# Performance work log

Hardware: AMD Instinct MI355X
Metric: run time of the kernel (lower is better)

## Reference

```python
import jax, jax.numpy as jnp
import numpy as np

N_NODES = 50000
N_EDGES = 500000
IN_F, HID, EMB = 128, 256, 128

def setup_inputs() -> dict:
    key = jax.random.key(0)
    ks = jax.random.split(key, 9)
    x = jax.random.normal(ks[0], (N_NODES, IN_F), dtype=jnp.float32)
    src = jax.random.randint(ks[1], (N_EDGES,), 0, N_NODES, dtype=jnp.int32)
    dst = jax.random.randint(ks[2], (N_EDGES,), 0, N_NODES, dtype=jnp.int32)
    def lin(k, fan_in, fan_out):
        bound = 1.0 / np.sqrt(fan_in)
        kw, kb = jax.random.split(k)
        W = jax.random.uniform(kw, (fan_in, fan_out), minval=-bound, maxval=bound, dtype=jnp.float32)
        b = jax.random.uniform(kb, (fan_out,), minval=-bound, maxval=bound, dtype=jnp.float32)
        return W, b
    W1, b1 = lin(ks[3], IN_F, HID)
    W2, b2 = lin(ks[4], HID, HID)
    W3, b3 = lin(ks[5], HID, EMB)
    return {"x": x, "src": src, "dst": dst, "W1": W1, "b1": b1,
            "W2": W2, "b2": b2, "W3": W3, "b3": b3}

def _gcn_layer(h, src, dst, W, b):
    # sum messages from src nodes into dst nodes, then linear
    agg = jax.ops.segment_sum(h[src], dst, num_segments=N_NODES)  # [N, F]
    return agg @ W + b

def reference(x, src, dst, W1, b1, W2, b2, W3, b3):
    h = jax.nn.relu(_gcn_layer(x, src, dst, W1, b1))
    h = jax.nn.relu(_gcn_layer(h, src, dst, W2, b2))
    h = _gcn_layer(h, src, dst, W3, b3)
    # dgl.mean_nodes on a single graph: mean of relu(h) over all nodes -> [EMB]
    return jnp.mean(jax.nn.relu(h), axis=0)
```

## Files before the change

kernel.cpp:

```cpp
#include <hip/hip_runtime.h>

#define N_NODES 50000
#define N_EDGES 500000

typedef __attribute__((ext_vector_type(8))) short short8;
typedef __attribute__((ext_vector_type(4))) float floatx4;

__device__ inline float bf2f(unsigned short u) {
    unsigned int x = ((unsigned int)u) << 16;
    return __builtin_bit_cast(float, x);
}
__device__ inline unsigned short f2bf(float f) {
    unsigned int x = __builtin_bit_cast(unsigned int, f);
    x += 0x7fff + ((x >> 16) & 1);
    return (unsigned short)(x >> 16);
}


__global__ void hist_kernel(const int* __restrict__ dst, int* __restrict__ deg, int nE) {
    int e = blockIdx.x * 256 + threadIdx.x;
    if (e < nE) atomicAdd(&deg[dst[e]], 1);
}

__global__ void scan_block_kernel(const int* __restrict__ deg, int* __restrict__ partial,
                                  int* __restrict__ bsum, int n) {
    __shared__ int s[256];
    int i = blockIdx.x * 256 + threadIdx.x;
    int v = (i < n) ? deg[i] : 0;
    s[threadIdx.x] = v;
    __syncthreads();
    #pragma unroll
    for (int d = 1; d < 256; d <<= 1) {
        int t = (threadIdx.x >= d) ? s[threadIdx.x - d] : 0;
        __syncthreads();
        s[threadIdx.x] += t;
        __syncthreads();
    }
    if (i < n) partial[i] = s[threadIdx.x];
    if (threadIdx.x == 255) bsum[blockIdx.x] = s[255];
}

__global__ void scan_bsum_kernel(int* __restrict__ bsum, int nb) {
    __shared__ int s[256];
    int t = threadIdx.x;
    int v = (t < nb) ? bsum[t] : 0;
    s[t] = v;
    __syncthreads();
    #pragma unroll
    for (int d = 1; d < 256; d <<= 1) {
        int u = (t >= d) ? s[t - d] : 0;
        __syncthreads();
        s[t] += u;
        __syncthreads();
    }
    if (t < nb) bsum[t] = s[t];
}

__global__ void finalize_kernel(const int* __restrict__ partial, const int* __restrict__ bsum,
                                int* __restrict__ cur, int* __restrict__ off, int n) {
    int i = blockIdx.x * 256 + threadIdx.x;
    if (i == 0) off[0] = 0;
    if (i < n) {
        int base = (blockIdx.x > 0) ? bsum[blockIdx.x - 1] : 0;
        int incl = base + partial[i];
        off[i + 1] = incl;
        cur[i] = incl - cur[i];
    }
}

__global__ void fill_kernel(const int* __restrict__ src, const int* __restrict__ dst,
                            int* __restrict__ cur, int* __restrict__ csr, int nE) {
    int e = blockIdx.x * 256 + threadIdx.x;
    if (e < nE) {
        int p = atomicAdd(&cur[dst[e]], 1);
        csr[p] = src[e];
    }
}


__global__ __launch_bounds__(256) void prep_kernel(const float* __restrict__ W1,
                                                   const float* __restrict__ W2,
                                                   const float* __restrict__ W3,
                                                   const float* __restrict__ x,
                                                   unsigned short* __restrict__ Wt1,
                                                   unsigned short* __restrict__ Wt2,
                                                   unsigned short* __restrict__ Wt3,
                                                   unsigned short* __restrict__ xb) {
    int idx = blockIdx.x * 256 + threadIdx.x;
    if (idx < 32768) {
        int k = idx >> 8, n = idx & 255;
        Wt1[n * 128 + k] = f2bf(W1[idx]);
    } else if (idx < 98304) {
        int i = idx - 32768;
        int k = i >> 8, n = i & 255;
        Wt2[n * 256 + k] = f2bf(W2[i]);
    } else if (idx < 131072) {
        int i = idx - 98304;
        int k = i >> 7, n = i & 127;
        Wt3[n * 256 + k] = f2bf(W3[i]);
    } else {
        int i = (idx - 131072) * 4;
        if (i < N_NODES * 128) {
            float4 v = *(const float4*)(x + i);
            ushort4 o;
            o.x = f2bf(v.x); o.y = f2bf(v.y); o.z = f2bf(v.z); o.w = f2bf(v.w);
            *(ushort4*)(xb + i) = o;
        }
    }
}


__global__ __launch_bounds__(256) void agg256_kernel(const unsigned short* __restrict__ h,
                                                     const int* __restrict__ off,
                                                     const int* __restrict__ csr,
                                                     unsigned short* __restrict__ outp) {
    int wave = threadIdx.x >> 6, lane = threadIdx.x & 63;
    int node = blockIdx.x * 4 + wave;
    int f0 = lane * 4;
    int s = __builtin_amdgcn_readfirstlane(off[node]);
    int e = __builtin_amdgcn_readfirstlane(off[node + 1]);
    float a0 = 0.f, a1 = 0.f, a2 = 0.f, a3 = 0.f;
    int i = s;
    for (; i + 8 <= e; i += 8) {
        ushort4 r[8];
        #pragma unroll
        for (int j = 0; j < 8; j++) {
            int id = csr[i + j];
            r[j] = *(const ushort4*)(h + (size_t)id * 256 + f0);
        }
        #pragma unroll
        for (int j = 0; j < 8; j++) {
            a0 += bf2f(r[j].x); a1 += bf2f(r[j].y);
            a2 += bf2f(r[j].z); a3 += bf2f(r[j].w);
        }
    }
    if (i < e) {
        ushort4 r[8];
        #pragma unroll
        for (int j = 0; j < 8; j++) {
            int ii = i + j;
            int id = csr[ii < e ? ii : e - 1];
            r[j] = *(const ushort4*)(h + (size_t)id * 256 + f0);
        }
        #pragma unroll
        for (int j = 0; j < 8; j++) {
            if (i + j < e) {
                a0 += bf2f(r[j].x); a1 += bf2f(r[j].y);
                a2 += bf2f(r[j].z); a3 += bf2f(r[j].w);
            }
        }
    }
    ushort4 o;
    o.x = f2bf(a0); o.y = f2bf(a1); o.z = f2bf(a2); o.w = f2bf(a3);
    *(ushort4*)(outp + (size_t)node * 256 + f0) = o;
}


__device__ inline void agg128_body(const unsigned short* __restrict__ h,
                                   const int* __restrict__ off,
                                   const int* __restrict__ csr,
                                   int node, int half, int f0,
                                   float& a0, float& a1, float& a2, float& a3) {
    int s = __builtin_amdgcn_readfirstlane(off[node]);
    int e = __builtin_amdgcn_readfirstlane(off[node + 1]);
    int i = s;
    for (; i + 8 <= e; i += 8) {
        ushort4 r[4];
        #pragma unroll
        for (int j = 0; j < 4; j++) {
            int i0 = csr[i + 2 * j];
            int i1 = csr[i + 2 * j + 1];
            int id = half ? i1 : i0;
            r[j] = *(const ushort4*)(h + (size_t)id * 128 + f0);
        }
        #pragma unroll
        for (int j = 0; j < 4; j++) {
            a0 += bf2f(r[j].x); a1 += bf2f(r[j].y);
            a2 += bf2f(r[j].z); a3 += bf2f(r[j].w);
        }
    }
    if (i < e) {
        ushort4 r[4];
        #pragma unroll
        for (int j = 0; j < 4; j++) {
            int c0 = i + 2 * j     < e ? i + 2 * j     : e - 1;
            int c1 = i + 2 * j + 1 < e ? i + 2 * j + 1 : e - 1;
            int i0 = csr[c0];
            int i1 = csr[c1];
            int id = half ? i1 : i0;
            r[j] = *(const ushort4*)(h + (size_t)id * 128 + f0);
        }
        #pragma unroll
        for (int j = 0; j < 4; j++) {
            if (i + 2 * j + half < e) {
                a0 += bf2f(r[j].x); a1 += bf2f(r[j].y);
                a2 += bf2f(r[j].z); a3 += bf2f(r[j].w);
            }
        }
    }
    a0 += __shfl_xor(a0, 32, 64);
    a1 += __shfl_xor(a1, 32, 64);
    a2 += __shfl_xor(a2, 32, 64);
    a3 += __shfl_xor(a3, 32, 64);
}

__global__ __launch_bounds__(256) void agg128_kernel(const unsigned short* __restrict__ h,
                                                     const int* __restrict__ off,
                                                     const int* __restrict__ csr,
                                                     unsigned short* __restrict__ outp) {
    int wave = threadIdx.x >> 6, lane = threadIdx.x & 63;
    int node = blockIdx.x * 4 + wave;
    int half = lane >> 5;
    int f0 = (lane & 31) * 4;
    float a0, a1, a2, a3;
    a0 = a1 = a2 = a3 = 0.f;
    agg128_body(h, off, csr, node, half, f0, a0, a1, a2, a3);
    if (half == 0) {
        ushort4 o;
        o.x = f2bf(a0); o.y = f2bf(a1); o.z = f2bf(a2); o.w = f2bf(a3);
        *(ushort4*)(outp + (size_t)node * 128 + f0) = o;
    }
}


__global__ __launch_bounds__(256) void agg3_mean_kernel(const unsigned short* __restrict__ t,
                                                        const int* __restrict__ off,
                                                        const int* __restrict__ csr,
                                                        const float* __restrict__ b3,
                                                        float* __restrict__ partial) {
    __shared__ float sm[4 * 128];
    int wave = threadIdx.x >> 6, lane = threadIdx.x & 63;
    int node = blockIdx.x * 4 + wave;
    int half = lane >> 5;
    int f0 = (lane & 31) * 4;
    float a0, a1, a2, a3;
    a0 = a1 = a2 = a3 = 0.f;
    agg128_body(t, off, csr, node, half, f0, a0, a1, a2, a3);
    if (half == 0) {
        float4 bias = *(const float4*)(b3 + f0);
        float4 v;
        v.x = fmaxf(a0 + bias.x, 0.f);
        v.y = fmaxf(a1 + bias.y, 0.f);
        v.z = fmaxf(a2 + bias.z, 0.f);
        v.w = fmaxf(a3 + bias.w, 0.f);
        *(float4*)&sm[wave * 128 + f0] = v;
    }
    __syncthreads();
    if (threadIdx.x < 128) {
        int f = threadIdx.x;
        float p = sm[f] + sm[128 + f] + sm[256 + f] + sm[384 + f];
        partial[(size_t)blockIdx.x * 128 + f] = p;
    }
}

__global__ __launch_bounds__(256) void mean_reduce_kernel(const float* __restrict__ partial,
                                                          float* __restrict__ outp, int nRows) {
    __shared__ float s[256];
    int f = threadIdx.x & 127, half = threadIdx.x >> 7;
    int chunk = (nRows + gridDim.x - 1) / gridDim.x;
    int r0 = blockIdx.x * chunk;
    int r1 = r0 + chunk < nRows ? r0 + chunk : nRows;
    float acc = 0.f;
    for (int r = r0 + half; r < r1; r += 2) acc += partial[(size_t)r * 128 + f];
    s[threadIdx.x] = acc;
    __syncthreads();
    if (half == 0) atomicAdd(&outp[f], (s[f] + s[f + 128]) * (1.0f / N_NODES));
}


template<typename T> __device__ inline void storeC(T* p, float v);
template<> __device__ inline void storeC<float>(float* p, float v) { *p = v; }
template<> __device__ inline void storeC<unsigned short>(unsigned short* p, float v) { *p = f2bf(v); }

template<typename OUT_T>
__global__ __launch_bounds__(256) void gemm_bf16_kernel(const unsigned short* __restrict__ A,
                                                        const unsigned short* __restrict__ Bt,
                                                        const float* __restrict__ bias,
                                                        OUT_T* __restrict__ C,
                                                        int M, int K, int N, int doRelu) {
    constexpr int BM = 128, BN = 128, BK = 32, LDA = BK + 8;
    __shared__ unsigned short As[BM * LDA];
    __shared__ unsigned short Bs[BN * LDA];
    int tid = threadIdx.x;
    int m0 = blockIdx.y * BM, n0 = blockIdx.x * BN;
    int wave = tid >> 6, lane = tid & 63;
    int wm = wave >> 1, wn = wave & 1;
    int mlane = lane & 15, kgrp = lane >> 4;

    floatx4 acc[4][4];
    #pragma unroll
    for (int i = 0; i < 4; i++)
        #pragma unroll
        for (int j = 0; j < 4; j++) acc[i][j] = (floatx4){0.f, 0.f, 0.f, 0.f};

    for (int k0 = 0; k0 < K; k0 += BK) {
        #pragma unroll
        for (int it = 0; it < 2; ++it) {
            int c = tid + it * 256;
            int r = c >> 2, cb = (c & 3) * 8;
            int rg = m0 + r;
            short8 v;
            if (rg < M) v = *(const short8*)(A + (size_t)rg * K + k0 + cb);
            else        v = (short8){0, 0, 0, 0, 0, 0, 0, 0};
            *(short8*)&As[r * LDA + cb] = v;
            short8 w = *(const short8*)(Bt + (size_t)(n0 + r) * K + k0 + cb);
            *(short8*)&Bs[r * LDA + cb] = w;
        }
        __syncthreads();
        short8 af[4], bfr[4];
        #pragma unroll
        for (int mt = 0; mt < 4; mt++)
            af[mt] = *(const short8*)&As[(wm * 64 + mt * 16 + mlane) * LDA + kgrp * 8];
        #pragma unroll
        for (int nt = 0; nt < 4; nt++)
            bfr[nt] = *(const short8*)&Bs[(wn * 64 + nt * 16 + mlane) * LDA + kgrp * 8];
        #pragma unroll
        for (int mt = 0; mt < 4; mt++)
            #pragma unroll
            for (int nt = 0; nt < 4; nt++)
                acc[mt][nt] = __builtin_amdgcn_mfma_f32_16x16x32_bf16(af[mt], bfr[nt],
                                                                      acc[mt][nt], 0, 0, 0);
        __syncthreads();
    }
    #pragma unroll
    for (int mt = 0; mt < 4; mt++) {
        #pragma unroll
        for (int nt = 0; nt < 4; nt++) {
            int col = n0 + wn * 64 + nt * 16 + mlane;
            float bv = bias ? bias[col] : 0.f;
            #pragma unroll
            for (int r = 0; r < 4; r++) {
                int row = m0 + wm * 64 + mt * 16 + kgrp * 4 + r;
                if (row < M) {
                    float v = acc[mt][nt][r] + bv;
                    if (doRelu) v = fmaxf(v, 0.f);
                    storeC(C + (size_t)row * N + col, v);
                }
            }
        }
    }
}


extern "C" void kernel_launch(void* const* d_in, const int* in_sizes, int n_in,
                              void* d_out, int out_size, void* d_ws, size_t ws_size,
                              hipStream_t stream) {
    const float* x   = (const float*)d_in[0];
    const int*   src = (const int*)d_in[1];
    const int*   dst = (const int*)d_in[2];
    const float* W1 = (const float*)d_in[3];
    const float* b1 = (const float*)d_in[4];
    const float* W2 = (const float*)d_in[5];
    const float* b2 = (const float*)d_in[6];
    const float* W3 = (const float*)d_in[7];
    const float* b3 = (const float*)d_in[8];
    float* out = (float*)d_out;

    char* ws = (char*)d_ws;
    size_t o = 0;
    auto alloc = [&](size_t bytes) -> char* {
        char* p = ws + o;
        o = (o + bytes + 255) & ~(size_t)255;
        return p;
    };
    int* off     = (int*)alloc((size_t)(N_NODES + 1) * 4);
    int* cur     = (int*)alloc((size_t)N_NODES * 4);
    int* csr     = (int*)alloc((size_t)N_EDGES * 4);
    int* partial = (int*)alloc((size_t)N_NODES * 4);
    int* bsum    = (int*)alloc(256 * 4);
    unsigned short* Wt1 = (unsigned short*)alloc((size_t)128 * 256 * 2);
    unsigned short* Wt2 = (unsigned short*)alloc((size_t)256 * 256 * 2);
    unsigned short* Wt3 = (unsigned short*)alloc((size_t)256 * 128 * 2);
    char* R1 = alloc((size_t)N_NODES * 256 * 2);
    char* R2 = alloc((size_t)N_NODES * 256 * 2);
    char* R3 = alloc((size_t)N_NODES * 256 * 2);

    unsigned short* xb    = (unsigned short*)R1;
    unsigned short* aggX  = (unsigned short*)R2;
    unsigned short* h1    = (unsigned short*)R3;
    unsigned short* agg2o = (unsigned short*)R1;
    unsigned short* h2    = (unsigned short*)R2;
    unsigned short* t     = (unsigned short*)R3;
    float*          pmean = (float*)R1;

    const int nb = (N_NODES + 255) / 256;

    hipMemsetAsync(cur, 0, (size_t)N_NODES * 4, stream);
    hist_kernel<<<(N_EDGES + 255) / 256, 256, 0, stream>>>(dst, cur, N_EDGES);
    scan_block_kernel<<<nb, 256, 0, stream>>>(cur, partial, bsum, N_NODES);
    scan_bsum_kernel<<<1, 256, 0, stream>>>(bsum, nb);
    finalize_kernel<<<nb, 256, 0, stream>>>(partial, bsum, cur, off, N_NODES);
    fill_kernel<<<(N_EDGES + 255) / 256, 256, 0, stream>>>(src, dst, cur, csr, N_EDGES);

    const int prepThreads = 131072 + N_NODES * 128 / 4;
    prep_kernel<<<(prepThreads + 255) / 256, 256, 0, stream>>>(W1, W2, W3, x,
                                                               Wt1, Wt2, Wt3, xb);

    const int mb = (N_NODES + 127) / 128;

    agg128_kernel<<<N_NODES / 4, 256, 0, stream>>>(xb, off, csr, aggX);
    gemm_bf16_kernel<unsigned short><<<dim3(2, mb), 256, 0, stream>>>(aggX, Wt1, b1, h1,
                                                                      N_NODES, 128, 256, 1);
    agg256_kernel<<<N_NODES / 4, 256, 0, stream>>>(h1, off, csr, agg2o);
    gemm_bf16_kernel<unsigned short><<<dim3(2, mb), 256, 0, stream>>>(agg2o, Wt2, b2, h2,
                                                                      N_NODES, 256, 256, 1);
    gemm_bf16_kernel<unsigned short><<<dim3(1, mb), 256, 0, stream>>>(h2, Wt3, nullptr, t,
                                                                      N_NODES, 256, 128, 0);
    agg3_mean_kernel<<<N_NODES / 4, 256, 0, stream>>>(t, off, csr, b3, pmean);

    hipMemsetAsync(out, 0, 128 * 4, stream);
    mean_reduce_kernel<<<128, 256, 0, stream>>>(pmean, out, N_NODES / 4);
}
```

Before: 329.6 us.

## Widen aggregation gathers to 16-byte loads, fuse histogram into prep, widen GEMM N-tile

The aggregation kernels now have each lane load 8 bf16 values (16 bytes) per neighbour row and split edges across half-waves or quarter-waves, combining the partial sums with cross-lane shuffles. The intent is fewer, wider gather instructions and more edges in flight per wave. The degree histogram is merged into the weight/feature conversion kernel to save one launch. The first two GEMMs use a 256-wide N tile with 512 threads so each A tile is loaded once instead of twice, at the cost of half as many blocks and extra shuffle work in the aggregations.

```diff
diff --git a/kernel.cpp b/kernel.cpp
--- a/kernel.cpp
+++ b/kernel.cpp
@@ -4,6 +4,7 @@
 #define N_EDGES 500000
 
 typedef __attribute__((ext_vector_type(8))) short short8;
+typedef __attribute__((ext_vector_type(8))) unsigned short ushort8v;
 typedef __attribute__((ext_vector_type(4))) float floatx4;
 
 __device__ inline float bf2f(unsigned short u) {
@@ -16,11 +17,6 @@
     return (unsigned short)(x >> 16);
 }
 
-
-__global__ void hist_kernel(const int* __restrict__ dst, int* __restrict__ deg, int nE) {
-    int e = blockIdx.x * 256 + threadIdx.x;
-    if (e < nE) atomicAdd(&deg[dst[e]], 1);
-}
 
 __global__ void scan_block_kernel(const int* __restrict__ deg, int* __restrict__ partial,
                                   int* __restrict__ bsum, int n) {
@@ -78,15 +74,19 @@
 }
 
 
-__global__ __launch_bounds__(256) void prep_kernel(const float* __restrict__ W1,
-                                                   const float* __restrict__ W2,
-                                                   const float* __restrict__ W3,
-                                                   const float* __restrict__ x,
-                                                   unsigned short* __restrict__ Wt1,
-                                                   unsigned short* __restrict__ Wt2,
-                                                   unsigned short* __restrict__ Wt3,
-                                                   unsigned short* __restrict__ xb) {
+__global__ __launch_bounds__(256) void histprep_kernel(const int* __restrict__ dst,
+                                                       int* __restrict__ deg,
+                                                       const float* __restrict__ W1,
+                                                       const float* __restrict__ W2,
+                                                       const float* __restrict__ W3,
+                                                       const float* __restrict__ x,
+                                                       unsigned short* __restrict__ Wt1,
+                                                       unsigned short* __restrict__ Wt2,
+                                                       unsigned short* __restrict__ Wt3,
+                                                       unsigned short* __restrict__ xb) {
     int idx = blockIdx.x * 256 + threadIdx.x;
+    if (idx < N_EDGES) { atomicAdd(&deg[dst[idx]], 1); return; }
+    idx -= N_EDGES;
     if (idx < 32768) {
         int k = idx >> 8, n = idx & 255;
         Wt1[n * 128 + k] = f2bf(W1[idx]);
@@ -116,92 +116,104 @@
                                                      unsigned short* __restrict__ outp) {
     int wave = threadIdx.x >> 6, lane = threadIdx.x & 63;
     int node = blockIdx.x * 4 + wave;
-    int f0 = lane * 4;
+    int half = lane >> 5;
+    int f0 = (lane & 31) * 8;
     int s = __builtin_amdgcn_readfirstlane(off[node]);
     int e = __builtin_amdgcn_readfirstlane(off[node + 1]);
-    float a0 = 0.f, a1 = 0.f, a2 = 0.f, a3 = 0.f;
+    float a[8];
+    #pragma unroll
+    for (int k = 0; k < 8; k++) a[k] = 0.f;
     int i = s;
     for (; i + 8 <= e; i += 8) {
-        ushort4 r[8];
-        #pragma unroll
-        for (int j = 0; j < 8; j++) {
-            int id = csr[i + j];
-            r[j] = *(const ushort4*)(h + (size_t)id * 256 + f0);
-        }
-        #pragma unroll
-        for (int j = 0; j < 8; j++) {
-            a0 += bf2f(r[j].x); a1 += bf2f(r[j].y);
-            a2 += bf2f(r[j].z); a3 += bf2f(r[j].w);
-        }
+        ushort8v r[4];
+        #pragma unroll
+        for (int j = 0; j < 4; j++) {
+            int i0 = csr[i + 2 * j];
+            int i1 = csr[i + 2 * j + 1];
+            int id = half ? i1 : i0;
+            r[j] = *(const ushort8v*)(h + (size_t)id * 256 + f0);
+        }
+        #pragma unroll
+        for (int j = 0; j < 4; j++)
+            #pragma unroll
+            for (int k = 0; k < 8; k++) a[k] += bf2f(r[j][k]);
     }
     if (i < e) {
-        ushort4 r[8];
-        #pragma unroll
-        for (int j = 0; j < 8; j++) {
-            int ii = i + j;
-            int id = csr[ii < e ? ii : e - 1];
-            r[j] = *(const ushort4*)(h + (size_t)id * 256 + f0);
-        }
-        #pragma unroll
-        for (int j = 0; j < 8; j++) {
-            if (i + j < e) {
-                a0 += bf2f(r[j].x); a1 += bf2f(r[j].y);
-                a2 += bf2f(r[j].z); a3 += bf2f(r[j].w);
+        ushort8v r[4];
+        #pragma unroll
+        for (int j = 0; j < 4; j++) {
+            int b0 = i + 2 * j, b1 = i + 2 * j + 1;
+            int i0 = csr[b0 < e ? b0 : e - 1];
+            int i1 = csr[b1 < e ? b1 : e - 1];
+            int id = half ? i1 : i0;
+            r[j] = *(const ushort8v*)(h + (size_t)id * 256 + f0);
+        }
+        #pragma unroll
+        for (int j = 0; j < 4; j++) {
+            if (i + 2 * j + half < e) {
+                #pragma unroll
+                for (int k = 0; k < 8; k++) a[k] += bf2f(r[j][k]);
             }
         }
     }
-    ushort4 o;
-    o.x = f2bf(a0); o.y = f2bf(a1); o.z = f2bf(a2); o.w = f2bf(a3);
-    *(ushort4*)(outp + (size_t)node * 256 + f0) = o;
+    #pragma unroll
+    for (int k = 0; k < 8; k++) a[k] += __shfl_xor(a[k], 32, 64);
+    if (half == 0) {
+        ushort8v o;
+        #pragma unroll
+        for (int k = 0; k < 8; k++) o[k] = f2bf(a[k]);
+        *(ushort8v*)(outp + (size_t)node * 256 + f0) = o;
+    }
 }
 
 
 __device__ inline void agg128_body(const unsigned short* __restrict__ h,
                                    const int* __restrict__ off,
                                    const int* __restrict__ csr,
-                                   int node, int half, int f0,
-                                   float& a0, float& a1, float& a2, float& a3) {
+                                   int node, int quad, int f0, float* a) {
     int s = __builtin_amdgcn_readfirstlane(off[node]);
     int e = __builtin_amdgcn_readfirstlane(off[node + 1]);
     int i = s;
     for (; i + 8 <= e; i += 8) {
-        ushort4 r[4];
-        #pragma unroll
-        for (int j = 0; j < 4; j++) {
-            int i0 = csr[i + 2 * j];
-            int i1 = csr[i + 2 * j + 1];
-            int id = half ? i1 : i0;
-            r[j] = *(const ushort4*)(h + (size_t)id * 128 + f0);
-        }
-        #pragma unroll
-        for (int j = 0; j < 4; j++) {
-            a0 += bf2f(r[j].x); a1 += bf2f(r[j].y);
-            a2 += bf2f(r[j].z); a3 += bf2f(r[j].w);
-        }
+        ushort8v r[2];
+        #pragma unroll
+        for (int j = 0; j < 2; j++) {
+            int base = i + 4 * j;
+            int i0 = csr[base], i1 = csr[base + 1], i2 = csr[base + 2], i3 = csr[base + 3];
+            int id = quad == 0 ? i0 : quad == 1 ? i1 : quad == 2 ? i2 : i3;
+            r[j] = *(const ushort8v*)(h + (size_t)id * 128 + f0);
+        }
+        #pragma unroll
+        for (int j = 0; j < 2; j++)
+            #pragma unroll
+            for (int k = 0; k < 8; k++) a[k] += bf2f(r[j][k]);
     }
     if (i < e) {
-        ushort4 r[4];
-        #pragma unroll
-        for (int j = 0; j < 4; j++) {
-            int c0 = i + 2 * j     < e ? i + 2 * j     : e - 1;
-            int c1 = i + 2 * j + 1 < e ? i + 2 * j + 1 : e - 1;
-            int i0 = csr[c0];
-            int i1 = csr[c1];
-            int id = half ? i1 : i0;
-            r[j] = *(const ushort4*)(h + (size_t)id * 128 + f0);
-        }
-        #pragma unroll
-        for (int j = 0; j < 4; j++) {
-            if (i + 2 * j + half < e) {
-                a0 += bf2f(r[j].x); a1 += bf2f(r[j].y);
-                a2 += bf2f(r[j].z); a3 += bf2f(r[j].w);
+        ushort8v r[2];
+        #pragma unroll
+        for (int j = 0; j < 2; j++) {
+            int base = i + 4 * j;
+            int c0 = base < e ? base : e - 1;
+            int c1 = base + 1 < e ? base + 1 : e - 1;
+            int c2 = base + 2 < e ? base + 2 : e - 1;
+            int c3 = base + 3 < e ? base + 3 : e - 1;
+            int i0 = csr[c0], i1 = csr[c1], i2 = csr[c2], i3 = csr[c3];
+            int id = quad == 0 ? i0 : quad == 1 ? i1 : quad == 2 ? i2 : i3;
+            r[j] = *(const ushort8v*)(h + (size_t)id * 128 + f0);
+        }
+        #pragma unroll
+        for (int j = 0; j < 2; j++) {
+            if (i + 4 * j + quad < e) {
+                #pragma unroll
+                for (int k = 0; k < 8; k++) a[k] += bf2f(r[j][k]);
             }
         }
     }
-    a0 += __shfl_xor(a0, 32, 64);
-    a1 += __shfl_xor(a1, 32, 64);
-    a2 += __shfl_xor(a2, 32, 64);
-    a3 += __shfl_xor(a3, 32, 64);
+    #pragma unroll
+    for (int k = 0; k < 8; k++) {
+        a[k] += __shfl_xor(a[k], 16, 64);
+        a[k] += __shfl_xor(a[k], 32, 64);
+    }
 }
 
 __global__ __launch_bounds__(256) void agg128_kernel(const unsigned short* __restrict__ h,
@@ -210,15 +222,17 @@
                                                      unsigned short* __restrict__ outp) {
     int wave = threadIdx.x >> 6, lane = threadIdx.x & 63;
     int node = blockIdx.x * 4 + wave;
-    int half = lane >> 5;
-    int f0 = (lane & 31) * 4;
-    float a0, a1, a2, a3;
-    a0 = a1 = a2 = a3 = 0.f;
-    agg128_body(h, off, csr, node, half, f0, a0, a1, a2, a3);
-    if (half == 0) {
-        ushort4 o;
-        o.x = f2bf(a0); o.y = f2bf(a1); o.z = f2bf(a2); o.w = f2bf(a3);
-        *(ushort4*)(outp + (size_t)node * 128 + f0) = o;
+    int quad = lane >> 4;
+    int f0 = (lane & 15) * 8;
+    float a[8];
+    #pragma unroll
+    for (int k = 0; k < 8; k++) a[k] = 0.f;
+    agg128_body(h, off, csr, node, quad, f0, a);
+    if (quad == 0) {
+        ushort8v o;
+        #pragma unroll
+        for (int k = 0; k < 8; k++) o[k] = f2bf(a[k]);
+        *(ushort8v*)(outp + (size_t)node * 128 + f0) = o;
     }
 }
 
@@ -231,19 +245,16 @@
     __shared__ float sm[4 * 128];
     int wave = threadIdx.x >> 6, lane = threadIdx.x & 63;
     int node = blockIdx.x * 4 + wave;
-    int half = lane >> 5;
-    int f0 = (lane & 31) * 4;
-    float a0, a1, a2, a3;
-    a0 = a1 = a2 = a3 = 0.f;
-    agg128_body(t, off, csr, node, half, f0, a0, a1, a2, a3);
-    if (half == 0) {
-        float4 bias = *(const float4*)(b3 + f0);
-        float4 v;
-        v.x = fmaxf(a0 + bias.x, 0.f);
-        v.y = fmaxf(a1 + bias.y, 0.f);
-        v.z = fmaxf(a2 + bias.z, 0.f);
-        v.w = fmaxf(a3 + bias.w, 0.f);
-        *(float4*)&sm[wave * 128 + f0] = v;
+    int quad = lane >> 4;
+    int f0 = (lane & 15) * 8;
+    float a[8];
+    #pragma unroll
+    for (int k = 0; k < 8; k++) a[k] = 0.f;
+    agg128_body(t, off, csr, node, quad, f0, a);
+    if (quad == 0) {
+        #pragma unroll
+        for (int k = 0; k < 8; k++)
+            sm[wave * 128 + f0 + k] = fmaxf(a[k] + b3[f0 + k], 0.f);
     }
     __syncthreads();
     if (threadIdx.x < 128) {
@@ -272,19 +283,20 @@
 template<> __device__ inline void storeC<float>(float* p, float v) { *p = v; }
 template<> __device__ inline void storeC<unsigned short>(unsigned short* p, float v) { *p = f2bf(v); }
 
-template<typename OUT_T>
-__global__ __launch_bounds__(256) void gemm_bf16_kernel(const unsigned short* __restrict__ A,
-                                                        const unsigned short* __restrict__ Bt,
-                                                        const float* __restrict__ bias,
-                                                        OUT_T* __restrict__ C,
-                                                        int M, int K, int N, int doRelu) {
-    constexpr int BM = 128, BN = 128, BK = 32, LDA = BK + 8;
+template<int BN, typename OUT_T>
+__global__ __launch_bounds__(2 * BN) void gemm_bf16_kernel(const unsigned short* __restrict__ A,
+                                                           const unsigned short* __restrict__ Bt,
+                                                           const float* __restrict__ bias,
+                                                           OUT_T* __restrict__ C,
+                                                           int M, int K, int N, int doRelu) {
+    constexpr int BM = 128, BK = 32, LDA = BK + 8;
+    constexpr int T = 2 * BN;
     __shared__ unsigned short As[BM * LDA];
     __shared__ unsigned short Bs[BN * LDA];
     int tid = threadIdx.x;
     int m0 = blockIdx.y * BM, n0 = blockIdx.x * BN;
     int wave = tid >> 6, lane = tid & 63;
-    int wm = wave >> 1, wn = wave & 1;
+    int wm = wave & 1, wn = wave >> 1;
     int mlane = lane & 15, kgrp = lane >> 4;
 
     floatx4 acc[4][4];
@@ -295,14 +307,17 @@
 
     for (int k0 = 0; k0 < K; k0 += BK) {
         #pragma unroll
-        for (int it = 0; it < 2; ++it) {
-            int c = tid + it * 256;
+        for (int c = tid; c < 512; c += T) {
             int r = c >> 2, cb = (c & 3) * 8;
             int rg = m0 + r;
             short8 v;
             if (rg < M) v = *(const short8*)(A + (size_t)rg * K + k0 + cb);
             else        v = (short8){0, 0, 0, 0, 0, 0, 0, 0};
             *(short8*)&As[r * LDA + cb] = v;
+        }
+        #pragma unroll
+        for (int c = tid; c < BN * 4; c += T) {
+            int r = c >> 2, cb = (c & 3) * 8;
             short8 w = *(const short8*)(Bt + (size_t)(n0 + r) * K + k0 + cb);
             *(short8*)&Bs[r * LDA + cb] = w;
         }
@@ -386,26 +401,24 @@
     const int nb = (N_NODES + 255) / 256;
 
     hipMemsetAsync(cur, 0, (size_t)N_NODES * 4, stream);
-    hist_kernel<<<(N_EDGES + 255) / 256, 256, 0, stream>>>(dst, cur, N_EDGES);
+    const int hpThreads = N_EDGES + 131072 + N_NODES * 128 / 4;
+    histprep_kernel<<<(hpThreads + 255) / 256, 256, 0, stream>>>(dst, cur, W1, W2, W3, x,
+                                                                 Wt1, Wt2, Wt3, xb);
     scan_block_kernel<<<nb, 256, 0, stream>>>(cur, partial, bsum, N_NODES);
     scan_bsum_kernel<<<1, 256, 0, stream>>>(bsum, nb);
     finalize_kernel<<<nb, 256, 0, stream>>>(partial, bsum, cur, off, N_NODES);
     fill_kernel<<<(N_EDGES + 255) / 256, 256, 0, stream>>>(src, dst, cur, csr, N_EDGES);
 
-    const int prepThreads = 131072 + N_NODES * 128 / 4;
-    prep_kernel<<<(prepThreads + 255) / 256, 256, 0, stream>>>(W1, W2, W3, x,
-                                                               Wt1, Wt2, Wt3, xb);
-
     const int mb = (N_NODES + 127) / 128;
 
     agg128_kernel<<<N_NODES / 4, 256, 0, stream>>>(xb, off, csr, aggX);
-    gemm_bf16_kernel<unsigned short><<<dim3(2, mb), 256, 0, stream>>>(aggX, Wt1, b1, h1,
-                                                                      N_NODES, 128, 256, 1);
+    gemm_bf16_kernel<256, unsigned short><<<dim3(1, mb), 512, 0, stream>>>(aggX, Wt1, b1, h1,
+                                                                           N_NODES, 128, 256, 1);
     agg256_kernel<<<N_NODES / 4, 256, 0, stream>>>(h1, off, csr, agg2o);
-    gemm_bf16_kernel<unsigned short><<<dim3(2, mb), 256, 0, stream>>>(agg2o, Wt2, b2, h2,
-                                                                      N_NODES, 256, 256, 1);
-    gemm_bf16_kernel<unsigned short><<<dim3(1, mb), 256, 0, stream>>>(h2, Wt3, nullptr, t,
-                                                                      N_NODES, 256, 128, 0);
+    gemm_bf16_kernel<256, unsigned short><<<dim3(1, mb), 512, 0, stream>>>(agg2o, Wt2, b2, h2,
+                                                                           N_NODES, 256, 256, 1);
+    gemm_bf16_kernel<128, unsigned short><<<dim3(1, mb), 256, 0, stream>>>(h2, Wt3, nullptr, t,
+                                                                           N_NODES, 256, 128, 0);
     agg3_mean_kernel<<<N_NODES / 4, 256, 0, stream>>>(t, off, csr, b3, pmean);
 
     hipMemsetAsync(out, 0, 128 * 4, stream);
```

New measurement: 307.4 us. -6.7%, faster.
